# Optimization experiments

Measured on AMD Instinct MI355X. Metric: run time of the kernel, lower is better.

Reference implementation:

```python
import jax, jax.numpy as jnp
import numpy as np

N_NODES = 100000
N_EDGES = 1600000
NUM_GRAPHS = 4096
HID = 128
F_IN = 11
F_OUT = 19


def setup_inputs() -> dict:
    key = jax.random.key(0)
    ks = jax.random.split(key, 8)
    x = jax.random.normal(ks[0], (N_NODES, F_IN), dtype=jnp.float32)
    edge_src = jax.random.randint(ks[1], (N_EDGES,), 0, N_NODES)
    edge_dst = jax.random.randint(ks[2], (N_EDGES,), 0, N_NODES)
    batch = jnp.sort(jax.random.randint(ks[3], (N_NODES,), 0, NUM_GRAPHS))
    W1 = jax.random.normal(ks[4], (F_IN, HID), dtype=jnp.float32) / np.sqrt(F_IN)
    b1 = jnp.zeros((HID,), dtype=jnp.float32)
    W2 = jax.random.normal(ks[5], (HID, HID), dtype=jnp.float32) / np.sqrt(HID)
    b2 = jnp.zeros((HID,), dtype=jnp.float32)
    Wlin = jax.random.normal(ks[6], (HID, F_OUT), dtype=jnp.float32) / np.sqrt(HID)
    blin = jnp.zeros((F_OUT,), dtype=jnp.float32)
    return {"x": x, "edge_src": edge_src, "edge_dst": edge_dst, "batch": batch,
            "W1": W1, "b1": b1, "W2": W2, "b2": b2, "Wlin": Wlin, "blin": blin}


def _gcn_conv(x, W, b, src, dst, norm, n_nodes):
    # x: [N, Fin] -> h: [N, Fout]; gather-normalize-scatter over edges (self-loops included in src/dst/norm)
    h = x @ W
    msgs = h[src] * norm[:, None]              # [E+N, Fout]
    out = jax.ops.segment_sum(msgs, dst, num_segments=n_nodes)
    return out + b


def reference(x, edge_src, edge_dst, batch, W1, b1, W2, b2, Wlin, blin):
    n = x.shape[0]
    # add self-loops (GCNConv default)
    loops = jnp.arange(n)
    src = jnp.concatenate([edge_src, loops])
    dst = jnp.concatenate([edge_dst, loops])
    # symmetric normalization deg^-1/2[src] * deg^-1/2[dst], deg computed on dst with self-loops
    deg = jax.ops.segment_sum(jnp.ones_like(dst, dtype=x.dtype), dst, num_segments=n)
    dinv = jnp.where(deg > 0, jax.lax.rsqrt(deg), 0.0)
    norm = dinv[src] * dinv[dst]
    h = _gcn_conv(x, W1, b1, src, dst, norm, n)
    h = jax.nn.relu(h)
    h = _gcn_conv(h, W2, b2, src, dst, norm, n)
    # global mean pool over batch assignment
    sums = jax.ops.segment_sum(h, batch, num_segments=NUM_GRAPHS)
    cnts = jax.ops.segment_sum(jnp.ones((n,), dtype=h.dtype), batch, num_segments=NUM_GRAPHS)
    pooled = sums / jnp.maximum(cnts, 1.0)[:, None]   # [NUM_GRAPHS, HID]
    return pooled @ Wlin + blin                       # [NUM_GRAPHS, F_OUT]
```

## Files before the change

### kernel.cpp

```cpp
#include <hip/hip_runtime.h>
#include <hip/hip_fp16.h>

#define N_NODES 100000
#define N_EDGES 1600000
#define NUM_G   4096
#define HID     128
#define F_IN    11
#define F_PAD   16
#define F_OUT   19

#define NB      256
#define KPB     391
#define BCAP    8192
#define GCAP    1024
#define P01_EPB 2048
#define NBLK_E  782
#define NGBB    16
#define NREG    8
#define REGW    12500
#define GPB     4
#define NAGG    782
#define CH_G    8

__device__ inline void acc_row_f16(float* acc, uint4 u, float w) {
    const __half2* hp = (const __half2*)&u;
#pragma unroll
    for (int i = 0; i < 4; ++i) {
        acc[2 * i]     += __half2float(__low2half(hp[i]))  * w;
        acc[2 * i + 1] += __half2float(__high2half(hp[i])) * w;
    }
}
__device__ inline void add_row_f16(float* acc, uint4 u) {
    const __half2* hp = (const __half2*)&u;
#pragma unroll
    for (int i = 0; i < 4; ++i) {
        acc[2 * i]     += __half2float(__low2half(hp[i]));
        acc[2 * i + 1] += __half2float(__high2half(hp[i]));
    }
}

__global__ void p1_place(const int* __restrict__ src, const int* __restrict__ dst,
                         const int* __restrict__ batch,
                         int* __restrict__ bcur, unsigned int* __restrict__ ebuf,
                         int* __restrict__ gb) {
    if (blockIdx.x >= NBLK_E) {
        int g = (blockIdx.x - NBLK_E) * 256 + threadIdx.x;
        if (g < NUM_G) {
            int lo = 0, hi = N_NODES;
            while (lo < hi) { int m = (lo + hi) >> 1; if (batch[m] < g) lo = m + 1; else hi = m; }
            gb[g] = lo;
            if (g == NUM_G - 1) gb[NUM_G] = N_NODES;
        }
        return;
    }
    __shared__ int h[NB];
    __shared__ int lbase[NB];
    __shared__ int gbase[NB];
    __shared__ int wsum4[4];
    __shared__ int total_s;
    __shared__ unsigned int stage[P01_EPB];
    __shared__ unsigned char sbuck[P01_EPB];
    int tid = threadIdx.x;
    h[tid] = 0;
    __syncthreads();
    unsigned int pk[8]; int bn[8];
    int b0 = blockIdx.x * P01_EPB;
    int e8 = b0 + tid * 8;
    if (e8 + 8 <= N_EDGES) {
        int4 s0 = *(const int4*)(src + e8);
        int4 s1 = *(const int4*)(src + e8 + 4);
        int4 d0 = *(const int4*)(dst + e8);
        int4 d1 = *(const int4*)(dst + e8 + 4);
        int ss[8] = { s0.x, s0.y, s0.z, s0.w, s1.x, s1.y, s1.z, s1.w };
        int dd[8] = { d0.x, d0.y, d0.z, d0.w, d1.x, d1.y, d1.z, d1.w };
#pragma unroll
        for (int k = 0; k < 8; ++k) {
            bn[k] = dd[k] / KPB;
            pk[k] = ((unsigned)ss[k] << 9) | (unsigned)(dd[k] - bn[k] * KPB);
        }
    } else {
#pragma unroll
        for (int k = 0; k < 8; ++k) {
            int e = e8 + k;
            if (e < N_EDGES) {
                int d = dst[e];
                bn[k] = d / KPB;
                pk[k] = ((unsigned)src[e] << 9) | (unsigned)(d - bn[k] * KPB);
            } else bn[k] = -1;
        }
    }
#pragma unroll
    for (int k = 0; k < 8; ++k)
        if (bn[k] >= 0) atomicAdd(&h[bn[k]], 1);
    __syncthreads();
    int c = h[tid];
    gbase[tid] = c ? atomicAdd(&bcur[tid], c) : 0;
    int lane = tid & 63, wv = tid >> 6;
    int sv = c;
#pragma unroll
    for (int off = 1; off < 64; off <<= 1) {
        int n = __shfl_up(sv, off, 64);
        if (lane >= off) sv += n;
    }
    if (lane == 63) wsum4[wv] = sv;
    __syncthreads();
    int woff = 0;
    for (int w = 0; w < wv; ++w) woff += wsum4[w];
    int excl = sv - c + woff;
    lbase[tid] = excl;
    if (tid == NB - 1) total_s = excl + c;
    __syncthreads();
    h[tid] = 0;
    __syncthreads();
#pragma unroll
    for (int k = 0; k < 8; ++k) {
        if (bn[k] >= 0) {
            int r = atomicAdd(&h[bn[k]], 1);
            int p_ = lbase[bn[k]] + r;
            stage[p_] = pk[k];
            sbuck[p_] = (unsigned char)bn[k];
        }
    }
    __syncthreads();
    int total = total_s;
    for (int i = tid; i < total; i += NB) {
        int b = sbuck[i];
        ebuf[(size_t)b * BCAP + gbase[b] + (i - lbase[b])] = stage[i];
    }
}

__global__ void p2_build(const unsigned int* __restrict__ ebuf, const int* __restrict__ bcur,
                         const float* __restrict__ x,
                         int* __restrict__ row_ptr, int* __restrict__ deg,
                         uint2* __restrict__ cw,
                         float* __restrict__ dinv, __half* __restrict__ xp) {
    __shared__ int hist[512];
    __shared__ float ldinv[512];
    __shared__ int wsum[8];
    __shared__ int woff[8];
    __shared__ uint2 scw[BCAP];
    int b  = blockIdx.x;
    int t  = threadIdx.x;
    int dbase = b * KPB;
    int nd = N_NODES - dbase; if (nd > KPB) nd = KPB;
    if (t < 512) hist[t] = 0;
    __syncthreads();
    int e0 = b * BCAP;
    int e1 = e0 + bcur[b];
    for (int e = e0 + t; e < e1; e += 1024)
        atomicAdd(&hist[ebuf[e] & 511u], 1);
    __syncthreads();
    int v = 0, sv = 0;
    int lane = t & 63, wv = t >> 6;
    if (t < 512) {
        v = hist[t];
        sv = v;
#pragma unroll
        for (int off = 1; off < 64; off <<= 1) {
            int n = __shfl_up(sv, off, 64);
            if (lane >= off) sv += n;
        }
        if (lane == 63) wsum[wv] = sv;
    }
    __syncthreads();
    if (t == 0) {
        int run = 0;
#pragma unroll
        for (int w = 0; w < 8; ++w) { woff[w] = run; run += wsum[w]; }
    }
    __syncthreads();
    int excl = 0;
    if (t < 512) {
        excl = sv - v + woff[wv];
        float di = rsqrtf(1.0f + (float)v);
        ldinv[t] = di;
        if (t < nd) {
            row_ptr[dbase + t] = e0 + excl;
            deg[dbase + t]     = v;
            dinv[dbase + t]    = di;
        }
    }
    __syncthreads();
    if (t < 512) hist[t] = excl;
    __syncthreads();
    for (int e = e0 + t; e < e1; e += 1024) {
        unsigned int w = ebuf[e];
        int dl = (int)(w & 511u);
        int pos = atomicAdd(&hist[dl], 1);
        scw[pos] = make_uint2(w >> 9, __float_as_uint(ldinv[dl]));
    }
    __syncthreads();
    int cnt_ = e1 - e0;
    for (int i = t; i < cnt_; i += 1024)
        cw[e0 + i] = scw[i];
    for (int idx = t; idx < nd * F_PAD; idx += 1024) {
        int vl = idx >> 4, f = idx & 15;
        int gv = dbase + vl;
        xp[(size_t)gv * F_PAD + f] =
            __float2half_rn((f < F_IN) ? ldinv[vl] * x[(size_t)gv * F_IN + f] : 0.f);
    }
}

__global__ void agg_es8(const __half* __restrict__ xp, const int* __restrict__ row_ptr,
                        const int* __restrict__ deg, const uint2* __restrict__ cw,
                        const float* __restrict__ dinv,
                        const float* __restrict__ W1, const float* __restrict__ b1,
                        __half* __restrict__ Bh,
                        const int* __restrict__ gb,
                        uint2* __restrict__ ewp, int* __restrict__ gro) {
    __shared__ union SBuf {
        struct {
            float xs[128][F_PAD];
            float W1s[F_IN * HID];
            float b1s[HID];
            float ds[128];
        } a;
        struct {
            uint2 dat[GCAP];
            uint2 ord[GCAP];
            unsigned char reg[GCAP];
        } s;
    } sh;
    __shared__ int cnt[NREG];
    __shared__ int cur[NREG];
    __shared__ int stot;
    int tid = threadIdx.x;

    if (blockIdx.x < NAGG) {
        for (int i = tid; i < F_IN * HID; i += 256) sh.a.W1s[i] = W1[i];
        if (tid < HID) sh.a.b1s[tid] = b1[tid];
        const uint4* xp4 = (const uint4*)xp;
        int v0   = blockIdx.x * 128;
        int v    = v0 + (tid >> 1);
        int lane = tid & 1;
        if (v < N_NODES) {
            if (lane == 0) sh.a.ds[tid >> 1] = dinv[v];
            float a[8];
#pragma unroll
            for (int k = 0; k < 8; ++k) a[k] = 0.f;
            add_row_f16(a, xp4[(size_t)v * 2 + lane]);
            int j = row_ptr[v], end = j + deg[v];
            for (; j + 3 < end; j += 4) {
                int s0 = cw[j].x, s1 = cw[j + 1].x, s2 = cw[j + 2].x, s3 = cw[j + 3].x;
                uint4 u0 = xp4[(size_t)s0 * 2 + lane];
                uint4 u1 = xp4[(size_t)s1 * 2 + lane];
                uint4 u2 = xp4[(size_t)s2 * 2 + lane];
                uint4 u3 = xp4[(size_t)s3 * 2 + lane];
                add_row_f16(a, u0); add_row_f16(a, u1);
                add_row_f16(a, u2); add_row_f16(a, u3);
            }
            for (; j < end; ++j)
                add_row_f16(a, xp4[(size_t)cw[j].x * 2 + lane]);
#pragma unroll
            for (int k = 0; k < 8; ++k) sh.a.xs[tid >> 1][lane * 8 + k] = a[k];
        }
        __syncthreads();
        int jf   = tid & 127;
        int half = tid >> 7;
        float w[F_IN];
#pragma unroll
        for (int k = 0; k < F_IN; ++k) w[k] = sh.a.W1s[k * HID + jf];
        float bb = sh.a.b1s[jf];
        int nmax = N_NODES - v0; if (nmax > 128) nmax = 128;
        for (int n = half; n < nmax; n += 2) {
            const float4* xr = (const float4*)sh.a.xs[n];
            float4 x0 = xr[0], x1 = xr[1], x2 = xr[2];
            float a = x0.x * w[0] + x0.y * w[1] + x0.z * w[2] + x0.w * w[3]
                    + x1.x * w[4] + x1.y * w[5] + x1.z * w[6] + x1.w * w[7]
                    + x2.x * w[8] + x2.y * w[9] + x2.z * w[10];
            float dv = sh.a.ds[n];
            float h = fmaxf(dv * a + bb, 0.f);
            Bh[(size_t)(v0 + n) * HID + jf] = __float2half_rn(dv * h);
        }
    } else {
        int g = blockIdx.x - NAGG;
        if (tid < NREG) cnt[tid] = 0;
        if (tid == 0) stot = 0;
        __syncthreads();
        int r0 = gb[g], r1 = gb[g + 1];
        int bb0 = 0, bb1 = -1;
        if (r1 > r0) { bb0 = r0 / KPB; bb1 = (r1 - 1) / KPB; }
        for (int bb = bb0; bb <= bb1; ++bb) {
            int vlo = r0 > bb * KPB ? r0 : bb * KPB;
            int vhi = r1 < bb * KPB + KPB ? r1 : bb * KPB + KPB;
            int ee0 = row_ptr[vlo];
            int ee1 = row_ptr[vhi - 1] + deg[vhi - 1];
            for (int e = ee0 + tid; e < ee1; e += 256) {
                uint2 q = cw[e];
                int rg = (int)(q.x / REGW);
                int si = atomicAdd(&stot, 1);
                sh.s.dat[si] = q;
                sh.s.reg[si] = (unsigned char)rg;
                atomicAdd(&cnt[rg], 1);
            }
        }
        for (int v = r0 + tid; v < r1; v += 256) {
            int rg = (int)((unsigned)v / REGW);
            int si = atomicAdd(&stot, 1);
            sh.s.dat[si] = make_uint2((unsigned)v, __float_as_uint(dinv[v]));
            sh.s.reg[si] = (unsigned char)rg;
            atomicAdd(&cnt[rg], 1);
        }
        __syncthreads();
        if (tid == 0) {
            int run = 0;
#pragma unroll
            for (int p = 0; p < NREG; ++p) {
                gro[g * 9 + p] = g * GCAP + run;
                cur[p] = run;
                run += cnt[p];
            }
            gro[g * 9 + 8] = g * GCAP + run;
        }
        __syncthreads();
        int tot = stot;
        for (int i = tid; i < tot; i += 256) {
            int pos = atomicAdd(&cur[sh.s.reg[i]], 1);
            sh.s.ord[pos] = sh.s.dat[i];
        }
        __syncthreads();
        for (int i = tid; i < tot; i += 256)
            ewp[(size_t)g * GCAP + i] = sh.s.ord[i];
    }
}

__global__ void pool_gather(const __half* __restrict__ Bh,
                            const int* __restrict__ gro,
                            const uint2* __restrict__ ewp,
                            float* __restrict__ part) {
    __shared__ float red[32][HID + 4];
    int b    = blockIdx.x;
    int gset = b >> 3;
    int p    = b & 7;
    int tid  = threadIdx.x;
    int grp  = tid >> 3;
    int lane = tid & 7;
    int g    = gset * GPB + (grp >> 3);
    int q    = grp & 7;
    const uint4* B4 = (const uint4*)Bh;
    float acc[16];
#pragma unroll
    for (int k = 0; k < 16; ++k) acc[k] = 0.f;

    int e0 = gro[g * 9 + p], e1 = gro[g * 9 + p + 1];
    int e = e0 + q;
    for (; e + 8 < e1; e += 16) {
        uint2 q0 = ewp[e], q1 = ewp[e + 8];
        uint4 u00 = B4[(size_t)q0.x * 16 + lane];
        uint4 u01 = B4[(size_t)q0.x * 16 + 8 + lane];
        uint4 u10 = B4[(size_t)q1.x * 16 + lane];
        uint4 u11 = B4[(size_t)q1.x * 16 + 8 + lane];
        float w0 = __uint_as_float(q0.y), w1 = __uint_as_float(q1.y);
        acc_row_f16(acc,     u00, w0);
        acc_row_f16(acc + 8, u01, w0);
        acc_row_f16(acc,     u10, w1);
        acc_row_f16(acc + 8, u11, w1);
    }
    for (; e < e1; e += 8) {
        uint2 q0 = ewp[e];
        uint4 u00 = B4[(size_t)q0.x * 16 + lane];
        uint4 u01 = B4[(size_t)q0.x * 16 + 8 + lane];
        float w0 = __uint_as_float(q0.y);
        acc_row_f16(acc,     u00, w0);
        acc_row_f16(acc + 8, u01, w0);
    }
#pragma unroll
    for (int k = 0; k < 8; ++k) red[grp][lane * 8 + k]      = acc[k];
#pragma unroll
    for (int k = 0; k < 8; ++k) red[grp][64 + lane * 8 + k] = acc[8 + k];
    __syncthreads();
    for (int i = tid; i < GPB * HID; i += 256) {
        int gg = i >> 7, f = i & 127;
        int rb = gg * 8;
        float s = 0.f;
#pragma unroll
        for (int r = 0; r < 8; ++r) s += red[rb + r][f];
        part[(size_t)((gset * GPB + gg) * NREG + p) * HID + f] = s;
    }
}

__global__ void combine_head(const float* __restrict__ part, const int* __restrict__ gb,
                             const float* __restrict__ W2, const float* __restrict__ b2,
                             const float* __restrict__ Wlin, const float* __restrict__ blin,
                             float* __restrict__ out) {
    __shared__ float r[CH_G][HID];
    __shared__ float tt[CH_G][HID + 4];
    __shared__ float bsc[CH_G];
    int g0  = blockIdx.x * CH_G;
    int tid = threadIdx.x;
    int f   = tid & 127;
    int gh  = tid >> 7;
    int q0  = gh * 4;
#pragma unroll
    for (int c = 0; c < 4; ++c) {
        int gg = q0 + c;
        int g  = g0 + gg;
        float s = 0.f;
#pragma unroll
        for (int p = 0; p < NREG; ++p) s += part[(size_t)(g * NREG + p) * HID + f];
        int cnt = gb[g + 1] - gb[g];
        float inv = (cnt > 0) ? 1.0f / (float)cnt : 0.f;
        r[gg][f] = s * inv;
        if (f == 0) bsc[gg] = (cnt > 0) ? 1.0f : 0.f;
    }
    __syncthreads();
    float bf = b2[f];
    float t0 = bf * bsc[q0];
    float t1 = bf * bsc[q0 + 1];
    float t2 = bf * bsc[q0 + 2];
    float t3 = bf * bsc[q0 + 3];
#pragma unroll 4
    for (int k = 0; k < HID; ++k) {
        float w = W2[k * HID + f];
        t0 += r[q0][k] * w;
        t1 += r[q0 + 1][k] * w;
        t2 += r[q0 + 2][k] * w;
        t3 += r[q0 + 3][k] * w;
    }
    tt[q0][f]     = t0;
    tt[q0 + 1][f] = t1;
    tt[q0 + 2][f] = t2;
    tt[q0 + 3][f] = t3;
    __syncthreads();
    if (tid < CH_G * F_OUT) {
        int gg = tid / F_OUT;
        int fo = tid - gg * F_OUT;
        float o = blin[fo];
#pragma unroll 8
        for (int k = 0; k < HID; ++k) o += tt[gg][k] * Wlin[k * F_OUT + fo];
        out[(size_t)(g0 + gg) * F_OUT + fo] = o;
    }
}

extern "C" void kernel_launch(void* const* d_in, const int* in_sizes, int n_in,
                              void* d_out, int out_size, void* d_ws, size_t ws_size,
                              hipStream_t stream) {
    const float* x    = (const float*)d_in[0];
    const int*   esrc = (const int*)  d_in[1];
    const int*   edst = (const int*)  d_in[2];
    const int*   batch= (const int*)  d_in[3];
    const float* W1   = (const float*)d_in[4];
    const float* b1   = (const float*)d_in[5];
    const float* W2   = (const float*)d_in[6];
    const float* b2   = (const float*)d_in[7];
    const float* Wlin = (const float*)d_in[8];
    const float* blin = (const float*)d_in[9];
    float* out = (float*)d_out;

    char* p = (char*)d_ws;
    float*        dinv    = (float*)p;        p += sizeof(float) * N_NODES;
    __half*       xp      = (__half*)p;       p += sizeof(__half) * (size_t)N_NODES * F_PAD;
    __half*       Bh      = (__half*)p;       p += sizeof(__half) * (size_t)N_NODES * HID;
    unsigned int* ebuf    = (unsigned int*)p; p += sizeof(unsigned int) * (size_t)NB * BCAP;
    uint2*        cw      = (uint2*)p;        p += sizeof(uint2) * (size_t)NB * BCAP;
    int*          deg     = (int*)p;          p += sizeof(int) * N_NODES;
    uint2*        ewp     = (uint2*)p;        p += sizeof(uint2) * (size_t)NUM_G * GCAP;
    float*        part    = (float*)p;        p += sizeof(float) * (size_t)NUM_G * NREG * HID;
    int*          row_ptr = (int*)p;          p += sizeof(int) * (N_NODES + 4);
    int*          gb      = (int*)p;          p += sizeof(int) * (NUM_G + 4);
    int*          gro     = (int*)p;          p += sizeof(int) * (NUM_G * 9 + 4);
    int*          bcur    = (int*)p;          p += sizeof(int) * NB;

    hipMemsetAsync(bcur, 0, sizeof(int) * NB, stream);
    p1_place<<<NBLK_E + NGBB, 256, 0, stream>>>(esrc, edst, batch, bcur, ebuf, gb);
    p2_build<<<NB, 1024, 0, stream>>>(ebuf, bcur, x, row_ptr, deg, cw, dinv, xp);

    agg_es8<<<NAGG + NUM_G, 256, 0, stream>>>(xp, row_ptr, deg, cw, dinv, W1, b1, Bh,
                                              gb, ewp, gro);

    pool_gather<<<(NUM_G / GPB) * NREG, 256, 0, stream>>>(Bh, gro, ewp, part);

    combine_head<<<NUM_G / CH_G, 256, 0, stream>>>(part, gb, W2, b2, Wlin, blin, out);
}
```

Baseline: 202.9 us.

## Switch layer-1 aggregation to edge-parallel chunks with shared-memory atomics

Packs the local destination index into the upper bits of each CSR edge word, so edge chunks can identify their destination row. Layer-1 aggregation no longer gives each node a thread pair walking its own degree list. Each thread now takes 8 consecutive edges, accumulates runs that share a destination, and flushes them with shared-memory atomicAdd into the block's row buffer. This is meant to fix load imbalance from varying degrees and improve memory-level parallelism, at the cost of shared atomics and two 16-byte loads per edge per thread.

```diff
diff --git a/kernel.cpp b/kernel.cpp
--- a/kernel.cpp
+++ b/kernel.cpp
@@ -21,6 +21,8 @@
 #define GPB     4
 #define NAGG    782
 #define CH_G    8
+
+#define SRC_MASK 0x1FFFFu
 
 __device__ inline void acc_row_f16(float* acc, uint4 u, float w) {
     const __half2* hp = (const __half2*)&u;
@@ -187,7 +189,7 @@
         unsigned int w = ebuf[e];
         int dl = (int)(w & 511u);
         int pos = atomicAdd(&hist[dl], 1);
-        scw[pos] = make_uint2(w >> 9, __float_as_uint(ldinv[dl]));
+        scw[pos] = make_uint2(((w & 511u) << 17) | (w >> 9), __float_as_uint(ldinv[dl]));
     }
     __syncthreads();
     int cnt_ = e1 - e0;
@@ -208,7 +210,7 @@
                         __half* __restrict__ Bh,
                         const int* __restrict__ gb,
                         uint2* __restrict__ ewp, int* __restrict__ gro) {
-    __shared__ union SBuf {
+    __shared__ union __align__(16) SBuf {
         struct {
             float xs[128][F_PAD];
             float W1s[F_IN * HID];
@@ -222,7 +224,7 @@
         } s;
     } sh;
     __shared__ int cnt[NREG];
-    __shared__ int cur[NREG];
+    __shared__ int cur_s[NREG];
     __shared__ int stot;
     int tid = threadIdx.x;
 
@@ -231,28 +233,61 @@
         if (tid < HID) sh.a.b1s[tid] = b1[tid];
         const uint4* xp4 = (const uint4*)xp;
         int v0   = blockIdx.x * 128;
-        int v    = v0 + (tid >> 1);
-        int lane = tid & 1;
-        if (v < N_NODES) {
-            if (lane == 0) sh.a.ds[tid >> 1] = dinv[v];
-            float a[8];
-#pragma unroll
-            for (int k = 0; k < 8; ++k) a[k] = 0.f;
-            add_row_f16(a, xp4[(size_t)v * 2 + lane]);
-            int j = row_ptr[v], end = j + deg[v];
-            for (; j + 3 < end; j += 4) {
-                int s0 = cw[j].x, s1 = cw[j + 1].x, s2 = cw[j + 2].x, s3 = cw[j + 3].x;
-                uint4 u0 = xp4[(size_t)s0 * 2 + lane];
-                uint4 u1 = xp4[(size_t)s1 * 2 + lane];
-                uint4 u2 = xp4[(size_t)s2 * 2 + lane];
-                uint4 u3 = xp4[(size_t)s3 * 2 + lane];
-                add_row_f16(a, u0); add_row_f16(a, u1);
-                add_row_f16(a, u2); add_row_f16(a, u3);
+        int nmax = N_NODES - v0; if (nmax > 128) nmax = 128;
+        {
+            int n = tid >> 1, half = tid & 1;
+            if (n < nmax) {
+                float t8[8];
+#pragma unroll
+                for (int i = 0; i < 8; ++i) t8[i] = 0.f;
+                add_row_f16(t8, xp4[(size_t)(v0 + n) * 2 + half]);
+#pragma unroll
+                for (int i = 0; i < 8; ++i) sh.a.xs[n][half * 8 + i] = t8[i];
             }
-            for (; j < end; ++j)
-                add_row_f16(a, xp4[(size_t)cw[j].x * 2 + lane]);
-#pragma unroll
-            for (int k = 0; k < 8; ++k) sh.a.xs[tid >> 1][lane * 8 + k] = a[k];
+        }
+        if (tid < nmax) sh.a.ds[tid] = dinv[v0 + tid];
+        __syncthreads();
+        int bb0 = v0 / KPB;
+        int bb1 = (v0 + nmax - 1) / KPB;
+        for (int bb = bb0; bb <= bb1; ++bb) {
+            int vlo = v0 > bb * KPB ? v0 : bb * KPB;
+            int vhi = v0 + nmax < (bb + 1) * KPB ? v0 + nmax : (bb + 1) * KPB;
+            int ee0 = row_ptr[vlo];
+            int ee1 = row_ptr[vhi - 1] + deg[vhi - 1];
+            int nb0 = bb * KPB - v0;
+            for (int base = ee0 + tid * 8; base < ee1; base += 2048) {
+                int lim = ee1 - base; if (lim > 8) lim = 8;
+                float a[16];
+#pragma unroll
+                for (int k = 0; k < 16; ++k) a[k] = 0.f;
+                int cur = -1;
+                for (int k = 0; k < lim; ++k) {
+                    uint2 q = cw[base + k];
+                    int dl  = (int)(q.x >> 17);
+                    int s   = (int)(q.x & SRC_MASK);
+                    if (dl != cur) {
+                        if (cur >= 0) {
+                            int nblk = cur + nb0;
+#pragma unroll
+                            for (int f = 0; f < 16; ++f) {
+                                atomicAdd(&sh.a.xs[nblk][f], a[f]);
+                                a[f] = 0.f;
+                            }
+                        }
+                        cur = dl;
+                    }
+                    uint4 u0 = xp4[(size_t)s * 2];
+                    uint4 u1 = xp4[(size_t)s * 2 + 1];
+                    add_row_f16(a, u0);
+                    add_row_f16(a + 8, u1);
+                }
+                if (cur >= 0) {
+                    int nblk = cur + nb0;
+#pragma unroll
+                    for (int f = 0; f < 16; ++f)
+                        atomicAdd(&sh.a.xs[nblk][f], a[f]);
+                }
+            }
         }
         __syncthreads();
         int jf   = tid & 127;
@@ -260,16 +295,15 @@
         float w[F_IN];
 #pragma unroll
         for (int k = 0; k < F_IN; ++k) w[k] = sh.a.W1s[k * HID + jf];
-        float bb = sh.a.b1s[jf];
-        int nmax = N_NODES - v0; if (nmax > 128) nmax = 128;
+        float bb_ = sh.a.b1s[jf];
         for (int n = half; n < nmax; n += 2) {
             const float4* xr = (const float4*)sh.a.xs[n];
             float4 x0 = xr[0], x1 = xr[1], x2 = xr[2];
-            float a = x0.x * w[0] + x0.y * w[1] + x0.z * w[2] + x0.w * w[3]
-                    + x1.x * w[4] + x1.y * w[5] + x1.z * w[6] + x1.w * w[7]
-                    + x2.x * w[8] + x2.y * w[9] + x2.z * w[10];
+            float acc = x0.x * w[0] + x0.y * w[1] + x0.z * w[2] + x0.w * w[3]
+                      + x1.x * w[4] + x1.y * w[5] + x1.z * w[6] + x1.w * w[7]
+                      + x2.x * w[8] + x2.y * w[9] + x2.z * w[10];
             float dv = sh.a.ds[n];
-            float h = fmaxf(dv * a + bb, 0.f);
+            float h = fmaxf(dv * acc + bb_, 0.f);
             Bh[(size_t)(v0 + n) * HID + jf] = __float2half_rn(dv * h);
         }
     } else {
@@ -287,9 +321,10 @@
             int ee1 = row_ptr[vhi - 1] + deg[vhi - 1];
             for (int e = ee0 + tid; e < ee1; e += 256) {
                 uint2 q = cw[e];
-                int rg = (int)(q.x / REGW);
+                unsigned s = q.x & SRC_MASK;
+                int rg = (int)(s / REGW);
                 int si = atomicAdd(&stot, 1);
-                sh.s.dat[si] = q;
+                sh.s.dat[si] = make_uint2(s, q.y);
                 sh.s.reg[si] = (unsigned char)rg;
                 atomicAdd(&cnt[rg], 1);
             }
@@ -307,7 +342,7 @@
 #pragma unroll
             for (int p = 0; p < NREG; ++p) {
                 gro[g * 9 + p] = g * GCAP + run;
-                cur[p] = run;
+                cur_s[p] = run;
                 run += cnt[p];
             }
             gro[g * 9 + 8] = g * GCAP + run;
@@ -315,7 +350,7 @@
         __syncthreads();
         int tot = stot;
         for (int i = tid; i < tot; i += 256) {
-            int pos = atomicAdd(&cur[sh.s.reg[i]], 1);
+            int pos = atomicAdd(&cur_s[sh.s.reg[i]], 1);
             sh.s.ord[pos] = sh.s.dat[i];
         }
         __syncthreads();
```

Result: slower. 230.3 us (+13.5%).
